# Kernel tuning notes

Measured on AMD Instinct MI355X. Metric: run time of the kernel, lower is better.

## Reference

```python
import jax, jax.numpy as jnp
import numpy as np

B, N, D = 4, 4096, 1024
H, F = 16, 256
HD = D // H
EPS_ATTN = 1e-8
EPS_LN = 1e-5


def setup_inputs() -> dict:
    key = jax.random.key(0)
    ks = jax.random.split(key, 10)
    def kaiming(k, shape):
        fan_in = shape[1]
        return jax.random.normal(k, shape, jnp.float32) * jnp.sqrt(2.0 / fan_in)
    # orthogonal-ish random projection (plain gaussian init, then QR per head)
    pm = jax.random.normal(ks[0], (H, HD, F), jnp.float32)
    return {
        "x": jax.random.normal(ks[1], (B, N, D), jnp.float32),
        "proj": pm,
        "w_qkv": kaiming(ks[2], (3 * D, D)),
        "w_out": kaiming(ks[3], (D, D)),
        "b_out": jnp.zeros((D,), jnp.float32),
        "gamma": jnp.ones((D,), jnp.float32),
        "beta": jnp.zeros((D,), jnp.float32),
        "w1": kaiming(ks[4], (4 * D, D)),
        "b1": jnp.zeros((4 * D,), jnp.float32),
        "w2": kaiming(ks[5], (D, 4 * D)),
        "b2": jnp.zeros((D,), jnp.float32),
    }


def _layernorm(x, gamma, beta):
    mu = jnp.mean(x, axis=-1, keepdims=True)
    var = jnp.var(x, axis=-1, keepdims=True)
    return (x - mu) * jax.lax.rsqrt(var + EPS_LN) * gamma + beta


def reference(x, proj, w_qkv, w_out, b_out, gamma, beta, w1, b1, w2, b2):
    residual = x
    b, n, d = x.shape
    qkv = x @ w_qkv.T                      # (b,n,3d)
    q, k, v = jnp.split(qkv, 3, axis=-1)
    def to_heads(t):
        return t.reshape(b, n, H, HD).transpose(0, 2, 1, 3)  # (b,h,n,hd)
    q, k, v = to_heads(q), to_heads(k), to_heads(v)
    # kernel feature maps: elu(x)+1
    q_f = jax.nn.elu(jnp.einsum('bhnd,hdf->bhnf', q, proj)) + 1.0
    k_f = jax.nn.elu(jnp.einsum('bhnd,hdf->bhnf', k, proj)) + 1.0
    # non-causal FAVOR+ linear attention
    kv = jnp.einsum('bhnf,bhnd->bhfd', k_f, v)               # (b,h,f,hd)
    attn = jnp.einsum('bhnf,bhfd->bhnd', q_f, kv)            # (b,h,n,hd)
    k_sum = jnp.sum(k_f, axis=2)                             # (b,h,f)
    z = 1.0 / (jnp.einsum('bhnf,bhf->bhn', q_f, k_sum) + EPS_ATTN)
    attn = attn * z[..., None]
    attn = attn.transpose(0, 2, 1, 3).reshape(b, n, d)
    x = residual + attn @ w_out.T + b_out
    x = _layernorm(x, gamma, beta)
    h = jax.nn.gelu(x @ w1.T + b1, approximate=False)
    x = x + h @ w2.T + b2
    x = _layernorm(x, gamma, beta)
    return x
```

## Files before the change

kernel.cpp:

```cpp
#include <hip/hip_runtime.h>
#include <math.h>

typedef unsigned short u16;
typedef __bf16 bf16x8 __attribute__((ext_vector_type(8)));
typedef float f32x4 __attribute__((ext_vector_type(4)));
typedef unsigned short u16x4 __attribute__((ext_vector_type(4)));
typedef unsigned short u16x8 __attribute__((ext_vector_type(8)));

#define DEV static __device__ __forceinline__

DEV float bf2f(u16 u) { union { unsigned int i; float f; } x; x.i = ((unsigned int)u) << 16; return x.f; }
DEV u16 f2bf(float f) { union { float f; unsigned int i; } x; x.f = f; unsigned int r = x.i + 0x7fffu + ((x.i >> 16) & 1u); return (u16)(r >> 16); }

DEV void load_lds16(const void* g, void* l) {
  __builtin_amdgcn_global_load_lds((__attribute__((address_space(1))) void*)g,
                                   (__attribute__((address_space(3))) void*)l, 16, 0, 0);
}

DEV float gelu_tanh(float g) {
  float t = 0.7978845608f * g * (1.f + 0.044715f * g * g);
  return g / (1.f + __expf(-2.f * t));
}

template<int EPI>
__global__ __launch_bounds__(256, 2)
void gemm_nt(const u16* __restrict__ A, const u16* __restrict__ B, void* __restrict__ Cv,
             const float* __restrict__ aux0, const void* __restrict__ aux1,
             int M, int N, int K, int lda, int ldb, int ldc)
{
  __shared__ __align__(16) unsigned char smem[32768];
  const int tid = threadIdx.x;
  int bx = blockIdx.x, by = blockIdx.y;
  {
    const int GX = gridDim.x;
    const int nwg = GX * gridDim.y;
    if ((nwg & 7) == 0) {
      const int wg = by * GX + bx;
      const int cpx = nwg >> 3;
      const int xcd = wg & 7, s = wg >> 3;
      const int rows = cpx / GX;
      if ((GX & 7) == 0 && cpx == rows * GX && (rows & 7) == 0) {
        const int SC = GX >> 3;
        const int q = s >> 6, r = (s >> 3) & 7, c = s & 7;
        by = xcd * rows + (q / SC) * 8 + r;
        bx = (q % SC) * 8 + c;
      } else {
        const int swz = xcd * cpx + s;
        bx = swz % GX; by = swz / GX;
      }
    }
  }
  const int m0 = by * 128, n0 = bx * 128;
  const int wid = tid >> 6, lane = tid & 63;
  const int wr = wid >> 1, wc = wid & 1;
  const int ln15 = lane & 15, lq = lane >> 4;
  const int srow = tid >> 3, sch = tid & 7;

  f32x4 acc[4][4] = {};

  for (int k0 = 0; k0 < K; k0 += 64) {
#pragma unroll
    for (int i = 0; i < 4; ++i) {
      int r = i * 32 + srow;
      const unsigned char* src = (const unsigned char*)(A + (size_t)(m0 + r) * lda + k0) + ((sch ^ (r & 7)) << 4);
      load_lds16(src, smem + r * 128 + (sch << 4));
    }
#pragma unroll
    for (int i = 0; i < 4; ++i) {
      int r = i * 32 + srow;
      const unsigned char* src = (const unsigned char*)(B + (size_t)(n0 + r) * ldb + k0) + ((sch ^ (r & 7)) << 4);
      load_lds16(src, smem + 16384 + r * 128 + (sch << 4));
    }
    __syncthreads();
#pragma unroll
    for (int kk = 0; kk < 2; ++kk) {
      bf16x8 af[4], bfv[4];
#pragma unroll
      for (int m = 0; m < 4; ++m) {
        int r = wr * 64 + m * 16 + ln15;
        int kc = kk * 4 + lq;
        af[m] = *(const bf16x8*)(smem + r * 128 + ((kc ^ (r & 7)) << 4));
      }
#pragma unroll
      for (int n = 0; n < 4; ++n) {
        int r = wc * 64 + n * 16 + ln15;
        int kc = kk * 4 + lq;
        bfv[n] = *(const bf16x8*)(smem + 16384 + r * 128 + ((kc ^ (r & 7)) << 4));
      }
#pragma unroll
      for (int m = 0; m < 4; ++m)
#pragma unroll
        for (int n = 0; n < 4; ++n)
          acc[m][n] = __builtin_amdgcn_mfma_f32_16x16x32_bf16(af[m], bfv[n], acc[m][n], 0, 0, 0);
    }
    __syncthreads();
  }

#pragma unroll
  for (int m = 0; m < 4; ++m) {
#pragma unroll
    for (int n = 0; n < 4; ++n) {
      int col = n0 + wc * 64 + n * 16 + ln15;
#pragma unroll
      for (int j = 0; j < 4; ++j) {
        int row = m0 + wr * 64 + m * 16 + lq * 4 + j;
        float v = acc[m][n][j];
        size_t idx = (size_t)row * ldc + col;
        if (EPI == 0) {
          ((u16*)Cv)[idx] = f2bf(v);
        } else if (EPI == 3) {
          ((float*)Cv)[idx] = v + aux0[col] + ((const float*)aux1)[idx];
        } else if (EPI == 4) {
          ((u16*)Cv)[idx] = f2bf(gelu_tanh(v + aux0[col]));
        } else if (EPI == 7) {
          ((float*)Cv)[idx] = v + aux0[col] + bf2f(((const u16*)aux1)[idx]);
        }
      }
    }
  }
}

__global__ __launch_bounds__(256, 2)
void fused_kv(const u16* __restrict__ qkv, const u16* __restrict__ projT,
              float* __restrict__ kvpart, float* __restrict__ ksumpart)
{
  __shared__ __align__(16) unsigned char ktS[2][8192];
  __shared__ __align__(16) unsigned char vtS[2][8192];
  __shared__ __align__(16) unsigned char kfS[32768];
  const int tid = threadIdx.x;
  const int bh = blockIdx.y, chunk = blockIdx.x;
  const int b = bh >> 4, h = bh & 15;
  const int wid = tid >> 6, lane = tid & 63;
  const int ln15 = lane & 15, lq = lane >> 4;
  const int vN = tid >> 2, vD = (tid & 3) * 16;
  const int vCn = vN >> 3, vWb = (vN & 7) * 2;

  bf16x8 pf[4][2];
#pragma unroll
  for (int m = 0; m < 4; ++m)
#pragma unroll
    for (int kk = 0; kk < 2; ++kk) {
      int f = wid * 64 + m * 16 + ln15;
      pf[m][kk] = *(const bf16x8*)(projT + (size_t)h * 16384 + (size_t)f * 64 + (kk * 4 + lq) * 8);
    }

  float ksum_r = 0.f;
  f32x4 acc2[4][4] = {};
  const int nbase = chunk * 512;

  {
    const u16* kg = qkv + ((size_t)b * 4096 + nbase) * 3072 + 1024 + h * 64;
#pragma unroll
    for (int i = 0; i < 2; ++i) {
      int c = i * 256 + tid; int r = c >> 3, ch = c & 7;
      load_lds16((const unsigned char*)(kg + (size_t)r * 3072) + ((ch ^ (r & 7)) << 4),
                 ktS[0] + r * 128 + ch * 16);
    }
    const u16* vg = qkv + ((size_t)b * 4096 + nbase + vN) * 3072 + 2048 + h * 64 + vD;
    u16x8 va = *(const u16x8*)vg;
    u16x8 vb = *(const u16x8*)(vg + 8);
#pragma unroll
    for (int j = 0; j < 8; ++j) {
      int d = vD + j;
      *(u16*)(vtS[0] + d * 128 + ((vCn ^ (d & 7)) << 4) + vWb) = va[j];
    }
#pragma unroll
    for (int j = 0; j < 8; ++j) {
      int d = vD + 8 + j;
      *(u16*)(vtS[0] + d * 128 + ((vCn ^ (d & 7)) << 4) + vWb) = vb[j];
    }
  }
  __syncthreads();

  for (int t = 0; t < 8; ++t) {
    const int cur = t & 1, nxt = cur ^ 1;
    u16x8 va, vb;
    const bool havenext = (t + 1 < 8);
    if (havenext) {
      int n1 = nbase + (t + 1) * 64;
      const u16* kg = qkv + ((size_t)b * 4096 + n1) * 3072 + 1024 + h * 64;
#pragma unroll
      for (int i = 0; i < 2; ++i) {
        int c = i * 256 + tid; int r = c >> 3, ch = c & 7;
        load_lds16((const unsigned char*)(kg + (size_t)r * 3072) + ((ch ^ (r & 7)) << 4),
                   ktS[nxt] + r * 128 + ch * 16);
      }
      const u16* vg = qkv + ((size_t)b * 4096 + n1 + vN) * 3072 + 2048 + h * 64 + vD;
      va = *(const u16x8*)vg;
      vb = *(const u16x8*)(vg + 8);
    }

    bf16x8 bvk[2][4];
#pragma unroll
    for (int kk = 0; kk < 2; ++kk)
#pragma unroll
      for (int n = 0; n < 4; ++n) {
        int r = n * 16 + ln15, kc = kk * 4 + lq;
        bvk[kk][n] = *(const bf16x8*)(ktS[cur] + r * 128 + ((kc ^ (r & 7)) << 4));
      }
#pragma unroll
    for (int m = 0; m < 4; ++m) {
      f32x4 a1[4] = {};
#pragma unroll
      for (int kk = 0; kk < 2; ++kk)
#pragma unroll
        for (int n = 0; n < 4; ++n)
          a1[n] = __builtin_amdgcn_mfma_f32_16x16x32_bf16(pf[m][kk], bvk[kk][n], a1[n], 0, 0, 0);
#pragma unroll
      for (int n = 0; n < 4; ++n) {
        int nloc = n * 16 + ln15;
        int c = nloc >> 3, wb = (nloc & 7) * 2;
#pragma unroll
        for (int j = 0; j < 4; ++j) {
          int f = wid * 64 + m * 16 + lq * 4 + j;
          float v = a1[n][j];
          float o = v > 0.f ? v + 1.f : __expf(v);
          *(u16*)(kfS + f * 128 + ((c ^ (f & 7)) << 4) + wb) = f2bf(o);
        }
      }
    }
    __syncthreads();

    {
      int f = tid;
      float s = 0.f;
#pragma unroll
      for (int c = 0; c < 8; ++c) {
        u16x8 v = *(const u16x8*)(kfS + f * 128 + ((c ^ (f & 7)) << 4));
#pragma unroll
        for (int j = 0; j < 8; ++j) s += bf2f(v[j]);
      }
      ksum_r += s;
    }
#pragma unroll
    for (int kk = 0; kk < 2; ++kk) {
      int kc = kk * 4 + lq;
      bf16x8 af[4], bv[4];
#pragma unroll
      for (int m = 0; m < 4; ++m) { int r = wid * 64 + m * 16 + ln15; af[m] = *(const bf16x8*)(kfS + r * 128 + ((kc ^ (r & 7)) << 4)); }
#pragma unroll
      for (int n = 0; n < 4; ++n) { int r = n * 16 + ln15; bv[n] = *(const bf16x8*)(vtS[cur] + r * 128 + ((kc ^ (r & 7)) << 4)); }
#pragma unroll
      for (int m = 0; m < 4; ++m)
#pragma unroll
        for (int n = 0; n < 4; ++n)
          acc2[m][n] = __builtin_amdgcn_mfma_f32_16x16x32_bf16(af[m], bv[n], acc2[m][n], 0, 0, 0);
    }
    if (havenext) {
#pragma unroll
      for (int j = 0; j < 8; ++j) {
        int d = vD + j;
        *(u16*)(vtS[nxt] + d * 128 + ((vCn ^ (d & 7)) << 4) + vWb) = va[j];
      }
#pragma unroll
      for (int j = 0; j < 8; ++j) {
        int d = vD + 8 + j;
        *(u16*)(vtS[nxt] + d * 128 + ((vCn ^ (d & 7)) << 4) + vWb) = vb[j];
      }
    }
    __syncthreads();
  }

  const size_t pbase = ((size_t)bh * 8 + chunk) * 16384;
#pragma unroll
  for (int half = 0; half < 2; ++half) {
#pragma unroll
    for (int m = 0; m < 4; ++m)
#pragma unroll
      for (int n2 = 0; n2 < 2; ++n2) {
        int n = half * 2 + n2;
        int dloc = n2 * 16 + ln15;
        int f = wid * 64 + m * 16 + lq * 4;
        *(f32x4*)(kfS + dloc * 1024 + ((f * 4) ^ ((dloc & 7) << 4))) = acc2[m][n];
      }
    __syncthreads();
#pragma unroll
    for (int k = 0; k < 8; ++k) {
      int dloc = k * 4 + wid;
      f32x4 val = *(const f32x4*)(kfS + dloc * 1024 + ((lane * 16) ^ ((dloc & 7) << 4)));
      *(f32x4*)(kvpart + pbase + (size_t)(half * 32 + dloc) * 256 + lane * 4) = val;
    }
    __syncthreads();
  }
  ksumpart[((size_t)bh * 8 + chunk) * 256 + tid] = ksum_r;
}

__global__ __launch_bounds__(256) void kv_finalize(const float* __restrict__ kvpart,
    const float* __restrict__ ksumpart, u16* __restrict__ kvT, float* __restrict__ ksum)
{
  int bx = blockIdx.x, bh = bx >> 2, dq = bx & 3, tid = threadIdx.x;
  const float* base = kvpart + (size_t)bh * 131072;
  u16* out = kvT + (size_t)bh * 16384;
#pragma unroll
  for (int k = 0; k < 16; ++k) {
    int idx = dq * 4096 + k * 256 + tid;
    float s = 0.f;
#pragma unroll
    for (int c = 0; c < 8; ++c) s += base[(size_t)c * 16384 + idx];
    out[idx] = f2bf(s);
  }
  if (dq == 0) {
    float s = 0.f;
#pragma unroll
    for (int c = 0; c < 8; ++c) s += ksumpart[((size_t)bh * 8 + c) * 256 + tid];
    ksum[(size_t)bh * 256 + tid] = s;
  }
}

__global__ __launch_bounds__(256, 3)
void fused_attn(const u16* __restrict__ qkv, const u16* __restrict__ projT,
                const u16* __restrict__ kvT, const float* __restrict__ ksum,
                u16* __restrict__ attnb)
{
  __shared__ __align__(16) unsigned char qtS[8192];
  __shared__ __align__(16) unsigned char qfS[32768];
  __shared__ float zpart[64][4];
  __shared__ float zS[64];
  const int tid = threadIdx.x;
  const int bh = blockIdx.y, nt = blockIdx.x;
  const int b = bh >> 4, h = bh & 15;
  const int wid = tid >> 6, lane = tid & 63;
  const int ln15 = lane & 15, lq = lane >> 4;
  const int n0 = nt * 64;

  bf16x8 pf[4][2];
#pragma unroll
  for (int n = 0; n < 4; ++n)
#pragma unroll
    for (int kk = 0; kk < 2; ++kk) {
      int f = wid * 64 + n * 16 + ln15;
      pf[n][kk] = *(const bf16x8*)(projT + (size_t)h * 16384 + (size_t)f * 64 + (kk * 4 + lq) * 8);
    }

  const u16* qg = qkv + ((size_t)b * 4096 + n0) * 3072 + h * 64;
#pragma unroll
  for (int i = 0; i < 2; ++i) {
    int c = i * 256 + tid; int r = c >> 3, ch = c & 7;
    load_lds16((const unsigned char*)(qg + (size_t)r * 3072) + ((ch ^ (r & 7)) << 4),
               qtS + r * 128 + ch * 16);
  }
  __syncthreads();

#pragma unroll
  for (int m = 0; m < 4; ++m) {
    bf16x8 af[2];
#pragma unroll
    for (int kk = 0; kk < 2; ++kk) {
      int r = m * 16 + ln15, kc = kk * 4 + lq;
      af[kk] = *(const bf16x8*)(qtS + r * 128 + ((kc ^ (r & 7)) << 4));
    }
    f32x4 a1[4] = {};
#pragma unroll
    for (int kk = 0; kk < 2; ++kk)
#pragma unroll
      for (int n = 0; n < 4; ++n)
        a1[n] = __builtin_amdgcn_mfma_f32_16x16x32_bf16(af[kk], pf[n][kk], a1[n], 0, 0, 0);
#pragma unroll
    for (int n = 0; n < 4; ++n) {
      int f = wid * 64 + n * 16 + ln15;
      int c = f >> 3, wb = (f & 7) * 2;
#pragma unroll
      for (int j = 0; j < 4; ++j) {
        int row = m * 16 + lq * 4 + j;
        float v = a1[n][j];
        float o = v > 0.f ? v + 1.f : __expf(v);
        *(u16*)(qfS + row * 512 + ((c ^ (row & 7)) << 4) + wb) = f2bf(o);
      }
    }
  }
  __syncthreads();

  {
    int n = tid & 63, q = tid >> 6;
    const float* kp = ksum + (size_t)bh * 256;
    float s = 0.f;
#pragma unroll
    for (int c = q * 8; c < q * 8 + 8; ++c) {
      u16x8 v = *(const u16x8*)(qfS + n * 512 + ((c ^ (n & 7)) << 4));
#pragma unroll
      for (int j = 0; j < 8; ++j) s += bf2f(v[j]) * kp[c * 8 + j];
    }
    zpart[n][q] = s;
  }
  __syncthreads();
  if (tid < 64) zS[tid] = 1.f / (zpart[tid][0] + zpart[tid][1] + zpart[tid][2] + zpart[tid][3] + 1e-8f);
  __syncthreads();

  f32x4 a2[4] = {};
  const u16* kvg = kvT + (size_t)bh * 16384;
#pragma unroll
  for (int kk = 0; kk < 8; ++kk) {
    int kc = kk * 4 + lq;
    int r = wid * 16 + ln15;
    bf16x8 af = *(const bf16x8*)(qfS + r * 512 + ((kc ^ (r & 7)) << 4));
#pragma unroll
    for (int nf = 0; nf < 4; ++nf) {
      int d = nf * 16 + ln15;
      bf16x8 bv = *(const bf16x8*)(kvg + (size_t)d * 256 + kc * 8);
      a2[nf] = __builtin_amdgcn_mfma_f32_16x16x32_bf16(af, bv, a2[nf], 0, 0, 0);
    }
  }
#pragma unroll
  for (int nf = 0; nf < 4; ++nf)
#pragma unroll
    for (int j = 0; j < 4; ++j) {
      int d = nf * 16 + ln15;
      int n = wid * 16 + lq * 4 + j;
      float v = a2[nf][j] * zS[n];
      attnb[((size_t)b * 4096 + n0 + n) * 1024 + h * 64 + d] = f2bf(v);
    }
}

__global__ __launch_bounds__(256) void cast_kernel(const float* __restrict__ in, u16* __restrict__ out, int n4)
{
  int i = blockIdx.x * 256 + threadIdx.x;
  if (i >= n4) return;
  float4 v = ((const float4*)in)[i];
  u16x4 o = { f2bf(v.x), f2bf(v.y), f2bf(v.z), f2bf(v.w) };
  ((u16x4*)out)[i] = o;
}

__global__ __launch_bounds__(256) void castw_kernel(const float* __restrict__ wqkv, const float* __restrict__ wout,
                                                    const float* __restrict__ w1, const float* __restrict__ w2,
                                                    u16* __restrict__ owqkv, u16* __restrict__ owout,
                                                    u16* __restrict__ ow1, u16* __restrict__ ow2)
{
  int bid = blockIdx.x;
  const float* src; u16* dst; int base;
  if (bid < 3072)      { src = wqkv; dst = owqkv; base = bid; }
  else if (bid < 4096) { src = wout; dst = owout; base = bid - 3072; }
  else if (bid < 8192) { src = w1;   dst = ow1;   base = bid - 4096; }
  else                 { src = w2;   dst = ow2;   base = bid - 8192; }
  int i = base * 256 + threadIdx.x;
  float4 v = ((const float4*)src)[i];
  u16x4 o = { f2bf(v.x), f2bf(v.y), f2bf(v.z), f2bf(v.w) };
  ((u16x4*)dst)[i] = o;
}

__global__ __launch_bounds__(256) void projt_kernel(const float* __restrict__ proj, u16* __restrict__ out)
{
  int i = blockIdx.x * 256 + threadIdx.x;
  int d = i & 63, f = (i >> 6) & 255, h = i >> 14;
  out[i] = f2bf(proj[((size_t)h * 64 + d) * 256 + f]);
}

__global__ __launch_bounds__(256) void ln_kernel(const float* __restrict__ in, const float* __restrict__ gamma,
                                                 const float* __restrict__ beta, float* __restrict__ outF,
                                                 u16* __restrict__ outB)
{
  int row = blockIdx.x, tid = threadIdx.x;
  float4 v = ((const float4*)(in + (size_t)row * 1024))[tid];
  float s = v.x + v.y + v.z + v.w;
  float q = v.x * v.x + v.y * v.y + v.z * v.z + v.w * v.w;
  for (int off = 32; off; off >>= 1) { s += __shfl_down(s, off); q += __shfl_down(q, off); }
  __shared__ float rs[4], rq[4];
  int wid = tid >> 6, lane = tid & 63;
  if (!lane) { rs[wid] = s; rq[wid] = q; }
  __syncthreads();
  s = rs[0] + rs[1] + rs[2] + rs[3];
  q = rq[0] + rq[1] + rq[2] + rq[3];
  float mu = s * (1.f / 1024.f);
  float rstd = rsqrtf(q * (1.f / 1024.f) - mu * mu + 1e-5f);
  float4 g = ((const float4*)gamma)[tid];
  float4 bb = ((const float4*)beta)[tid];
  float4 o;
  o.x = (v.x - mu) * rstd * g.x + bb.x;
  o.y = (v.y - mu) * rstd * g.y + bb.y;
  o.z = (v.z - mu) * rstd * g.z + bb.z;
  o.w = (v.w - mu) * rstd * g.w + bb.w;
  if (outF) ((float4*)(outF + (size_t)row * 1024))[tid] = o;
  if (outB) {
    u16x4 ob = { f2bf(o.x), f2bf(o.y), f2bf(o.z), f2bf(o.w) };
    ((u16x4*)(outB + (size_t)row * 1024))[tid] = ob;
  }
}

#define O_WQKVB   0L
#define O_WOUTB   6291456L
#define O_W1B     8388608L
#define O_W2B     16777216L
#define O_PROJT   25165824L
#define O_KSUM    25690112L
#define O_KSP     26804224L
#define O_KVB     27852800L
#define O_QFG     37289984L
#define O_QKVB    70844416L
#define O_ATTNB   171507712L
#define WS_NEED   205062144L

extern "C" void kernel_launch(void* const* d_in, const int* in_sizes, int n_in,
                              void* d_out, int out_size, void* d_ws, size_t ws_size,
                              hipStream_t stream)
{
  if (ws_size < (size_t)WS_NEED) return;

  const float* x     = (const float*)d_in[0];
  const float* proj  = (const float*)d_in[1];
  const float* wqkv  = (const float*)d_in[2];
  const float* wout  = (const float*)d_in[3];
  const float* bout  = (const float*)d_in[4];
  const float* gamma = (const float*)d_in[5];
  const float* beta  = (const float*)d_in[6];
  const float* w1    = (const float*)d_in[7];
  const float* b1    = (const float*)d_in[8];
  const float* w2    = (const float*)d_in[9];
  const float* b2    = (const float*)d_in[10];
  float* outp = (float*)d_out;
  char* ws = (char*)d_ws;

  u16* wqkvb  = (u16*)(ws + O_WQKVB);
  u16* woutb  = (u16*)(ws + O_WOUTB);
  u16* w1b    = (u16*)(ws + O_W1B);
  u16* w2b    = (u16*)(ws + O_W2B);
  u16* projTb = (u16*)(ws + O_PROJT);
  float* ksumf= (float*)(ws + O_KSUM);
  float* ksp  = (float*)(ws + O_KSP);
  u16* kvTb   = (u16*)(ws + O_KVB);
  float* kvp  = (float*)(ws + O_QFG);
  u16* x1b    = (u16*)(ws + O_QFG);
  u16* qkvb   = (u16*)(ws + O_QKVB);
  float* tf   = (float*)(ws + O_QKVB);
  u16* hfull  = (u16*)(ws + O_QKVB);
  u16* attnb  = (u16*)(ws + O_ATTNB);

  u16* xbD = (u16*)d_out;

  cast_kernel<<<16384, 256, 0, stream>>>(x, xbD, 4194304);
  castw_kernel<<<12288, 256, 0, stream>>>(wqkv, wout, w1, w2, wqkvb, woutb, w1b, w2b);
  projt_kernel<<<1024, 256, 0, stream>>>(proj, projTb);

  gemm_nt<0><<<dim3(24, 128), 256, 0, stream>>>(xbD, wqkvb, qkvb, nullptr, nullptr,
      16384, 3072, 1024, 1024, 1024, 3072);

  fused_kv<<<dim3(8, 64), 256, 0, stream>>>(qkvb, projTb, kvp, ksp);
  kv_finalize<<<256, 256, 0, stream>>>(kvp, ksp, kvTb, ksumf);
  fused_attn<<<dim3(64, 64), 256, 0, stream>>>(qkvb, projTb, kvTb, ksumf, attnb);

  gemm_nt<7><<<dim3(8, 128), 256, 0, stream>>>(attnb, woutb, tf, bout, xbD,
      16384, 1024, 1024, 1024, 1024, 1024);

  ln_kernel<<<16384, 256, 0, stream>>>(tf, gamma, beta, nullptr, x1b);

  gemm_nt<4><<<dim3(32, 128), 256, 0, stream>>>(x1b, w1b, hfull, b1, nullptr,
      16384, 4096, 1024, 1024, 1024, 4096);

  gemm_nt<7><<<dim3(8, 128), 256, 0, stream>>>(hfull, w2b, outp, b2, x1b,
      16384, 1024, 4096, 4096, 4096, 1024);

  ln_kernel<<<16384, 256, 0, stream>>>(outp, gamma, beta, outp, nullptr);
}
```

Before: 656.8 us.

## Add 256x256-tile 8-wave GEMM kernel for QKV and FFN-up projections

Adds a new bf16 MFMA GEMM kernel with 256x256 output tiles, 512 threads, and 128KB of LDS used as a double buffer with XOR swizzling. Loads are staged directly into LDS and interleaved with MFMA quarter-blocks, using barriers and s_setprio to overlap copies with compute. The QKV projection and the first FFN GEMM (gelu epilogue) switch to this kernel to raise arithmetic intensity and cut global and LDS traffic. The cost is one workgroup per CU and a large accumulator register footprint. The epilogue writes scalar, uncoalesced stores, and the 12x64 QKV grid falls back to a simpler XCD remap.

```diff
diff --git a/kernel.cpp b/kernel.cpp
--- a/kernel.cpp
+++ b/kernel.cpp
@@ -2,6 +2,7 @@
 #include <math.h>
 
 typedef unsigned short u16;
+typedef unsigned char u8;
 typedef __bf16 bf16x8 __attribute__((ext_vector_type(8)));
 typedef float f32x4 __attribute__((ext_vector_type(4)));
 typedef unsigned short u16x4 __attribute__((ext_vector_type(4)));
@@ -20,6 +21,151 @@
 DEV float gelu_tanh(float g) {
   float t = 0.7978845608f * g * (1.f + 0.044715f * g * g);
   return g / (1.f + __expf(-2.f * t));
+}
+
+#define MMAQ(AREG, BREG, MH, NH)                                                            \
+  do {                                                                                      \
+    __builtin_amdgcn_s_setprio(1);                                                          \
+    _Pragma("unroll") for (int m_ = 0; m_ < 4; ++m_)                                        \
+      _Pragma("unroll") for (int n_ = 0; n_ < 2; ++n_)                                      \
+        _Pragma("unroll") for (int kk_ = 0; kk_ < 2; ++kk_)                                 \
+          acc[(MH)*4 + m_][(NH)*2 + n_] = __builtin_amdgcn_mfma_f32_16x16x32_bf16(          \
+              AREG[m_][kk_], BREG[n_][kk_], acc[(MH)*4 + m_][(NH)*2 + n_], 0, 0, 0);        \
+    __builtin_amdgcn_s_setprio(0);                                                          \
+  } while (0)
+
+template<int EPI>
+__global__ __launch_bounds__(512, 1)
+void gemm256(const u16* __restrict__ A, const u16* __restrict__ B, void* __restrict__ Cv,
+             const float* __restrict__ aux0, const void* __restrict__ aux1,
+             int M, int N, int K, int lda, int ldb, int ldc)
+{
+  __shared__ __align__(16) unsigned char smem[131072];
+  const int tid = threadIdx.x;
+  int bx = blockIdx.x, by = blockIdx.y;
+  {
+    const int GX = gridDim.x;
+    const int nwg = GX * gridDim.y;
+    if ((nwg & 7) == 0) {
+      const int wg = by * GX + bx;
+      const int cpx = nwg >> 3;
+      const int xcd = wg & 7, s = wg >> 3;
+      const int rows = cpx / GX;
+      if ((GX & 7) == 0 && cpx == rows * GX && (rows & 7) == 0) {
+        const int SC = GX >> 3;
+        const int q = s >> 6, r = (s >> 3) & 7, c = s & 7;
+        by = xcd * rows + (q / SC) * 8 + r;
+        bx = (q % SC) * 8 + c;
+      } else {
+        const int swz = xcd * cpx + s;
+        bx = swz % GX; by = swz / GX;
+      }
+    }
+  }
+  const int m0 = by * 256, n0 = bx * 256;
+  const int wid = tid >> 6, lane = tid & 63;
+  const int wr = wid >> 2, wc = wid & 3;
+  const int ln15 = lane & 15, lq = lane >> 4;
+  const int bhalf = wc >> 1;
+  const int sRow = tid >> 3, sCh = tid & 7;
+
+  f32x4 acc[8][4] = {};
+  bf16x8 aR[4][2], b0R[2][2], b1R[2][2];
+
+  const unsigned sc = (unsigned)((sCh ^ (sRow & 7)) << 4);
+  const u8* gA0a = (const u8*)(A + (size_t)(m0 +       sRow) * lda) + sc;
+  const u8* gA0b = (const u8*)(A + (size_t)(m0 +  64 + sRow) * lda) + sc;
+  const u8* gA1a = (const u8*)(A + (size_t)(m0 + 128 + sRow) * lda) + sc;
+  const u8* gA1b = (const u8*)(A + (size_t)(m0 + 192 + sRow) * lda) + sc;
+  const u8* gB0a = (const u8*)(B + (size_t)(n0 +       sRow) * ldb) + sc;
+  const u8* gB0b = (const u8*)(B + (size_t)(n0 +  64 + sRow) * ldb) + sc;
+  const u8* gB1a = (const u8*)(B + (size_t)(n0 + 128 + sRow) * ldb) + sc;
+  const u8* gB1b = (const u8*)(B + (size_t)(n0 + 192 + sRow) * ldb) + sc;
+  const unsigned tb = (unsigned)(sRow * 128 + sCh * 16);
+  const unsigned dA0 = tb, dA1 = tb + 16384, dB0 = tb + 65536, dB1 = tb + 81920;
+
+  auto STG2 = [&](const u8* pa, const u8* pb, unsigned dst, unsigned bo, int kt) {
+    load_lds16(pa + (size_t)kt * 128, smem + dst + bo);
+    load_lds16(pb + (size_t)kt * 128, smem + dst + bo + 8192);
+  };
+
+  const unsigned swk0 = (unsigned)((lq ^ (ln15 & 7)) << 4);
+  const unsigned swk1 = (unsigned)(((4 + lq) ^ (ln15 & 7)) << 4);
+  const unsigned aOff0 = (unsigned)(wr * 16384 + ln15 * 128) + swk0;
+  const unsigned aOff1 = (unsigned)(wr * 16384 + ln15 * 128) + swk1;
+  const unsigned bOff0 = (unsigned)(65536 + bhalf * 16384 + ((wc & 1) * 64 + ln15) * 128) + swk0;
+  const unsigned bOff1 = (unsigned)(65536 + bhalf * 16384 + ((wc & 1) * 64 + ln15) * 128) + swk1;
+#define LDA(BO, MH)                                                                     \
+  do { _Pragma("unroll") for (int m_ = 0; m_ < 4; ++m_) {                               \
+    aR[m_][0] = *(const bf16x8*)(smem + aOff0 + (BO) + ((MH) * 8192 + m_ * 2048));      \
+    aR[m_][1] = *(const bf16x8*)(smem + aOff1 + (BO) + ((MH) * 8192 + m_ * 2048));      \
+  } } while (0)
+#define LDB(BO, NH, BQ)                                                                 \
+  do { _Pragma("unroll") for (int n_ = 0; n_ < 2; ++n_) {                               \
+    BQ[n_][0] = *(const bf16x8*)(smem + bOff0 + (BO) + ((NH) * 4096 + n_ * 2048));      \
+    BQ[n_][1] = *(const bf16x8*)(smem + bOff1 + (BO) + ((NH) * 4096 + n_ * 2048));      \
+  } } while (0)
+
+  auto quad = [&](unsigned BO, int ktN, int mode) {
+    LDA(BO, 0); LDB(BO, 0, b0R);
+    __builtin_amdgcn_s_barrier();
+    MMAQ(aR, b0R, 0, 0);
+    __builtin_amdgcn_s_barrier();
+    LDB(BO, 1, b1R);
+    __builtin_amdgcn_s_barrier();
+    MMAQ(aR, b1R, 0, 1);
+    __builtin_amdgcn_s_barrier();
+    LDA(BO, 1);
+    if (mode == 0) STG2(gB0a, gB0b, dB0, BO, ktN);
+    __builtin_amdgcn_s_barrier();
+    MMAQ(aR, b0R, 1, 0);
+    __builtin_amdgcn_s_barrier();
+    if (mode == 0) {
+      STG2(gB1a, gB1b, dB1, BO, ktN);
+      STG2(gA0a, gA0b, dA0, BO, ktN);
+      STG2(gA1a, gA1b, dA1, BO, ktN);
+    }
+    MMAQ(aR, b1R, 1, 1);
+    if (mode == 0)      asm volatile("s_waitcnt vmcnt(8)" ::: "memory");
+    else if (mode == 1) asm volatile("s_waitcnt vmcnt(0)" ::: "memory");
+    __builtin_amdgcn_s_barrier();
+  };
+
+  const int nkt = K >> 6, nit = nkt >> 1;
+
+  STG2(gA0a, gA0b, dA0, 0, 0); STG2(gA1a, gA1b, dA1, 0, 0);
+  STG2(gB0a, gB0b, dB0, 0, 0); STG2(gB1a, gB1b, dB1, 0, 0);
+  STG2(gA0a, gA0b, dA0, 32768, 1); STG2(gA1a, gA1b, dA1, 32768, 1);
+  STG2(gB0a, gB0b, dB0, 32768, 1); STG2(gB1a, gB1b, dB1, 32768, 1);
+  asm volatile("s_waitcnt vmcnt(8)" ::: "memory");
+  __builtin_amdgcn_s_barrier();
+
+  for (int it = 0; it < nit; ++it) {
+    const bool st = (it + 1 < nit);
+    quad(0u,     2 * it + 2, st ? 0 : 1);
+    quad(32768u, 2 * it + 3, st ? 0 : 2);
+  }
+
+#pragma unroll
+  for (int m = 0; m < 8; ++m) {
+#pragma unroll
+    for (int n = 0; n < 4; ++n) {
+      int col = n0 + wc * 64 + n * 16 + ln15;
+#pragma unroll
+      for (int j = 0; j < 4; ++j) {
+        int row = m0 + wr * 128 + m * 16 + lq * 4 + j;
+        float v = acc[m][n][j];
+        size_t idx = (size_t)row * ldc + col;
+        if (EPI == 0) {
+          ((u16*)Cv)[idx] = f2bf(v);
+        } else if (EPI == 4) {
+          ((u16*)Cv)[idx] = f2bf(gelu_tanh(v + aux0[col]));
+        }
+      }
+    }
+  }
+#undef LDA
+#undef LDB
 }
 
 template<int EPI>
@@ -529,7 +675,7 @@
   castw_kernel<<<12288, 256, 0, stream>>>(wqkv, wout, w1, w2, wqkvb, woutb, w1b, w2b);
   projt_kernel<<<1024, 256, 0, stream>>>(proj, projTb);
 
-  gemm_nt<0><<<dim3(24, 128), 256, 0, stream>>>(xbD, wqkvb, qkvb, nullptr, nullptr,
+  gemm256<0><<<dim3(12, 64), 512, 0, stream>>>(xbD, wqkvb, qkvb, nullptr, nullptr,
       16384, 3072, 1024, 1024, 1024, 3072);
 
   fused_kv<<<dim3(8, 64), 256, 0, stream>>>(qkvb, projTb, kvp, ksp);
@@ -541,7 +687,7 @@
 
   ln_kernel<<<16384, 256, 0, stream>>>(tf, gamma, beta, nullptr, x1b);
 
-  gemm_nt<4><<<dim3(32, 128), 256, 0, stream>>>(x1b, w1b, hfull, b1, nullptr,
+  gemm256<4><<<dim3(16, 64), 512, 0, stream>>>(x1b, w1b, hfull, b1, nullptr,
       16384, 4096, 1024, 1024, 1024, 4096);
 
   gemm_nt<7><<<dim3(8, 128), 256, 0, stream>>>(hfull, w2b, outp, b2, x1b,
```

Measured after the change: 685.9 us. 1.04x slower.
